# Optimization experiments

Hardware: AMD Instinct MI355X
Metric: run time of the kernel (lower is better)

## Reference

```python
import jax, jax.numpy as jnp
import numpy as np

N = 100_000   # nodes
E = 600_000   # edges
D = 128       # embed_dim
G = 1000      # graphs (batch ids)
L = 3         # num_layers


def setup_inputs() -> dict:
    key = jax.random.key(0)
    ks = jax.random.split(key, 12)
    s = 1.0 / np.sqrt(D)
    return {
        "x": jax.random.normal(ks[0], (N, D), jnp.float32),
        "edge_index": jax.random.randint(ks[1], (2, E), 0, N),
        "batch": jnp.sort(jax.random.randint(ks[2], (N,), 0, G)),
        "mask": jax.random.randint(ks[3], (N,), 0, 2),
        # stacked GCNConv weights/biases (in=hidden=out=D)
        "gcn_w": jax.random.normal(ks[4], (L, D, D), jnp.float32) * s,
        "gcn_b": jnp.zeros((L, D), jnp.float32),
        # MLP head: Linear(D,D) -> ReLU -> Linear(D,1)
        "lin1_w": jax.random.normal(ks[5], (D, D), jnp.float32) * s,
        "lin1_b": jnp.zeros((D,), jnp.float32),
        "lin2_w": jax.random.normal(ks[6], (D,), jnp.float32) * s,
        "lin2_b": jnp.zeros((), jnp.float32),
    }


def gcn_forward(x, src, dst, gcn_w, gcn_b):
    # symmetric gcn_norm with self-loops: deg[i] = 1 + in-degree(i)
    deg = jax.ops.segment_sum(jnp.ones((E,), x.dtype), dst, num_segments=N) + 1.0
    dinv = jax.lax.rsqrt(deg)
    enorm = dinv[src] * dinv[dst]          # [E] edge normalization
    self_norm = (dinv * dinv)[:, None]     # [N,1] self-loop normalization
    h = x
    for l in range(L):
        h = h @ gcn_w[l]                   # [N,D]
        h = (jax.ops.segment_sum(h[src] * enorm[:, None], dst, num_segments=N)
             + h * self_norm)
        h = h + gcn_b[l]
        if l < L - 1:
            h = jax.nn.relu(h)  # (dropout inactive at inference)
    return h


def reference(x, edge_index, batch, mask, gcn_w, gcn_b, lin1_w, lin1_b, lin2_w, lin2_b):
    src, dst = edge_index[0], edge_index[1]
    h = gcn_forward(x, src, dst, gcn_w, gcn_b)
    # MLP head -> per-node score [N]
    s = jax.nn.relu(h @ lin1_w + lin1_b) @ lin2_w + lin2_b
    s = jnp.where(mask == 0, jnp.float32(-1e9), s)
    # per-graph (segment) softmax — fused replacement for the unique/batch loop
    m = jax.ops.segment_max(s, batch, num_segments=G)
    e = jnp.exp(s - m[batch])
    z = jax.ops.segment_sum(e, batch, num_segments=G)
    return e / z[batch]
```

## Files before the change

### kernel.cpp

```cpp
#include <hip/hip_runtime.h>
#include <hip/hip_bf16.h>

typedef unsigned int u32;
typedef unsigned short u16;
typedef __attribute__((ext_vector_type(8))) short bf16x8;
typedef __attribute__((ext_vector_type(4))) float f32x4;

__device__ __forceinline__ float u16tof(u16 u){ return __uint_as_float(((u32)u) << 16); }
__device__ __forceinline__ float lo16(u32 v){ return __uint_as_float(v << 16); }
__device__ __forceinline__ float hi16(u32 v){ return __uint_as_float(v & 0xffff0000u); }
__device__ __forceinline__ u16 ftobf(float f){
  u32 b = __float_as_uint(f);
  return (u16)((b + 0x7FFFu + ((b >> 16) & 1u)) >> 16);
}
__device__ __forceinline__ u32 pack2(float a, float b){
  return (u32)ftobf(a) | ((u32)ftobf(b) << 16);
}
__device__ __forceinline__ float ldf(const void* p, int i, int isbf){
  return isbf ? u16tof(((const u16*)p)[i]) : ((const float*)p)[i];
}

__global__ __launch_bounds__(256) void k_prep(const void* __restrict__ gw, const void* __restrict__ l1w,
                                              const void* __restrict__ x, u16* __restrict__ Wf,
                                              u16* __restrict__ Hb, int L, int n8, int cvtB, int goffB,
                                              const int* __restrict__ batch, int* __restrict__ goff,
                                              int N, int G,
                                              const int* __restrict__ dst, int* __restrict__ bcnt,
                                              int nE, int chunk, int* __restrict__ flag){
  __shared__ int sh[256];
  const int b = blockIdx.x;
  const int t = threadIdx.x;
  const int histStart = L + 1 + cvtB + goffB;

  if (b >= histStart){
    sh[t] = 0; __syncthreads();
    const int blk = b - histStart;
    const int e0 = blk * chunk, e1 = min(e0 + chunk, nE);
    for (int e = e0 + t; e < e1; e += 256) atomicAdd(&sh[dst[e] >> 9], 1);
    __syncthreads();
    if (sh[t] > 0) atomicAdd(&bcnt[t], sh[t]);
    return;
  }
  if (b >= L + 1 + cvtB){
    const int i = (b - (L + 1 + cvtB)) * 256 + t;
    if (i >= N) return;
    const int bt = batch[i];
    const int prev = (i == 0) ? -1 : batch[i - 1];
    for (int g = prev + 1; g <= bt; ++g) goff[g] = i;
    if (i == N - 1){ for (int g = bt + 1; g <= G; ++g) goff[g] = N; }
    return;
  }
  if (t == 0) sh[0] = 0;
  __syncthreads();
  if (b <= L){
    int local = 0;
    for (int i = t; i < 4096; i += 256){
      u32 e = (((const u32*)gw)[i] >> 7) & 0xFFu;
      if (e >= 100u && e < 127u) local++;
    }
    atomicAdd(&sh[0], local);
    __syncthreads();
    const int isbf = (sh[0] > 2048) ? 1 : 0;
    if (b == 0 && t == 0) *flag = isbf;

    const void* src = (b < L) ? gw : l1w;
    const int sbase = (b < L) ? b * 16384 : 0;
    u16* dstp = Wf + (size_t)b * 16384;
    for (int g = t; g < 2048; g += 256){
      const int tt = g >> 8, ks = (g >> 6) & 3, lane = g & 63;
      const int n = tt * 16 + (lane & 15);
      const int k0 = ks * 32 + ((lane >> 4) << 3);
      u16* d = dstp + (size_t)g * 8;
      #pragma unroll
      for (int j = 0; j < 8; ++j){
        d[j] = ftobf(ldf(src, sbase + (k0 + j) * 128 + n, isbf));
      }
    }
  } else {
    u32 e = (((const u32*)gw)[t] >> 7) & 0xFFu;
    atomicAdd(&sh[0], (e >= 100u && e < 127u) ? 1 : 0);
    __syncthreads();
    if (sh[0] > 128) return;
    const int i = (b - (L + 1)) * 256 + t;
    if (i >= n8) return;
    const float4 a = ((const float4*)x)[i * 2];
    const float4 c = ((const float4*)x)[i * 2 + 1];
    u16* o = Hb + (size_t)i * 8;
    o[0] = ftobf(a.x); o[1] = ftobf(a.y); o[2] = ftobf(a.z); o[3] = ftobf(a.w);
    o[4] = ftobf(c.x); o[5] = ftobf(c.y); o[6] = ftobf(c.z); o[7] = ftobf(c.w);
  }
}

__global__ __launch_bounds__(256) void k_bbscan(const int* __restrict__ bcnt, int* __restrict__ bb,
                                                int* __restrict__ bpos, int nE){
  __shared__ int sm[256];
  const int t = threadIdx.x;
  const int v = bcnt[t];
  sm[t] = v; __syncthreads();
  for (int off = 1; off < 256; off <<= 1){
    int a = (t >= off) ? sm[t - off] : 0;
    __syncthreads();
    sm[t] += a;
    __syncthreads();
  }
  const int ex = sm[t] - v;
  bb[t] = ex;
  bpos[t] = ex;
  if (t == 255) bb[256] = nE;
}

__global__ __launch_bounds__(256) void k_scatter(const int* __restrict__ src, const int* __restrict__ dst,
                                                 int* __restrict__ bpos, int2* __restrict__ tmpe,
                                                 int nE, int chunk){
  __shared__ int cnt[256];
  __shared__ int base[256];
  const int blk = blockIdx.x, t = threadIdx.x;
  cnt[t] = 0;
  __syncthreads();
  const int e0 = blk * chunk, e1 = min(e0 + chunk, nE);
  for (int e = e0 + t; e < e1; e += 256) atomicAdd(&cnt[dst[e] >> 9], 1);
  __syncthreads();
  if (cnt[t] > 0) base[t] = atomicAdd(&bpos[t], cnt[t]);
  __syncthreads();
  for (int e = e0 + t; e < e1; e += 256){
    const int d = dst[e];
    const int pos = atomicAdd(&base[d >> 9], 1);
    tmpe[pos] = make_int2(src[e], d);
  }
}

__global__ __launch_bounds__(256) void k_local(const int2* __restrict__ tmpe, const int* __restrict__ bb,
                                               int* __restrict__ boff, int* __restrict__ eid,
                                               float* __restrict__ dinv, int N, int nE, int nbkt){
  __shared__ int hcnt[512];
  __shared__ int hoff[512];
  const int b = blockIdx.x, t = threadIdx.x;
  const int n0 = b << 9;
  const int n1 = min(n0 + 512, N);
  const int nn = n1 - n0;
  const int e0 = bb[b], e1 = bb[b + 1];
  hcnt[t] = 0; hcnt[t + 256] = 0;
  __syncthreads();
  for (int e = e0 + t; e < e1; e += 256) atomicAdd(&hcnt[tmpe[e].y - n0], 1);
  __syncthreads();
  const int v0 = hcnt[t], v1 = hcnt[t + 256];
  hoff[t] = v0; hoff[t + 256] = v1;
  __syncthreads();
  for (int off = 1; off < 512; off <<= 1){
    int a0 = (t >= off) ? hoff[t - off] : 0;
    int a1 = (t + 256 >= off) ? hoff[t + 256 - off] : 0;
    __syncthreads();
    hoff[t] += a0; hoff[t + 256] += a1;
    __syncthreads();
  }
  const int ex0 = hoff[t] - v0 + e0;
  const int ex1 = hoff[t + 256] - v1 + e0;
  if (t < nn){       boff[n0 + t] = ex0;        dinv[n0 + t] = rsqrtf((float)v0 + 1.0f); }
  if (t + 256 < nn){ boff[n0 + t + 256] = ex1;  dinv[n0 + t + 256] = rsqrtf((float)v1 + 1.0f); }
  if (b == nbkt - 1 && t == 0) boff[N] = nE;
  __syncthreads();
  hoff[t] = ex0; hoff[t + 256] = ex1;
  __syncthreads();
  for (int e = e0 + t; e < e1; e += 256){
    const int2 pr = tmpe[e];
    const int pos = atomicAdd(&hoff[pr.y - n0], 1);
    eid[pos] = pr.x;
  }
}

__global__ __launch_bounds__(256) void k_mm(const void* __restrict__ X, const u16* __restrict__ Hb, int use_x,
                                            const u16* __restrict__ Wf, const float* __restrict__ dinv,
                                            u16* __restrict__ T, int n, const int* __restrict__ fl){
  __shared__ u16 smw[16384];
  const int isbf = *fl;
  const u16* A = (use_x && isbf) ? (const u16*)X : Hb;
  {
    const uint4* s = (const uint4*)Wf;
    uint4* d = (uint4*)smw;
    for (int i = threadIdx.x; i < 2048; i += 256) d[i] = s[i];
  }
  __syncthreads();

  const int wave = threadIdx.x >> 6, lane = threadIdx.x & 63;
  const int m0 = blockIdx.x * 64 + wave * 16;
  int arow = m0 + (lane & 15); if (arow > n - 1) arow = n - 1;
  const u16* aptr = A + (size_t)arow * 128 + ((lane >> 4) << 3);

  f32x4 acc[8];
  #pragma unroll
  for (int t = 0; t < 8; ++t) acc[t] = (f32x4){0.f, 0.f, 0.f, 0.f};

  #pragma unroll
  for (int ks = 0; ks < 4; ++ks){
    const bf16x8 a = *(const bf16x8*)(aptr + ks * 32);
    #pragma unroll
    for (int t = 0; t < 8; ++t){
      const bf16x8 b = *(const bf16x8*)(smw + (size_t)(((t * 4 + ks) * 64 + lane) * 8));
      acc[t] = __builtin_amdgcn_mfma_f32_16x16x32_bf16(a, b, acc[t], 0, 0, 0);
    }
  }
  __syncthreads();

  const int quad = lane >> 4, col0 = lane & 15;
  float dv[4];
  #pragma unroll
  for (int r = 0; r < 4; ++r){
    const int row = m0 + quad * 4 + r;
    dv[r] = (row < n) ? dinv[row] : 0.f;
  }
  u16* my = smw + wave * 2112;
  #pragma unroll
  for (int t = 0; t < 8; ++t){
    #pragma unroll
    for (int r = 0; r < 4; ++r){
      my[(quad * 4 + r) * 132 + t * 16 + col0] = ftobf(acc[t][r] * dv[r]);
    }
  }
  #pragma unroll
  for (int i = 0; i < 4; ++i){
    const int row = i * 4 + (lane >> 4);
    const int grow = m0 + row;
    const int c8 = (lane & 15) * 8;
    if (grow < n){
      const u16* s = &my[row * 132 + c8];
      uint2 lo = *(const uint2*)(s);
      uint2 hi = *(const uint2*)(s + 4);
      *(uint4*)&T[(size_t)grow * 128 + c8] = make_uint4(lo.x, lo.y, hi.x, hi.y);
    }
  }
}

__global__ __launch_bounds__(256) void k_mmhead(const u16* __restrict__ Hb, const u16* __restrict__ Wf,
                                                const void* __restrict__ b1, const void* __restrict__ w2,
                                                const void* __restrict__ b2, const int* __restrict__ mask,
                                                float* __restrict__ s, int n, const int* __restrict__ fl){
  __shared__ u16 smw[16384];
  const int isbf = *fl;
  {
    const uint4* sp = (const uint4*)Wf;
    uint4* d = (uint4*)smw;
    for (int i = threadIdx.x; i < 2048; i += 256) d[i] = sp[i];
  }
  __syncthreads();

  const int wave = threadIdx.x >> 6, lane = threadIdx.x & 63;
  const int m0 = blockIdx.x * 64 + wave * 16;
  int arow = m0 + (lane & 15); if (arow > n - 1) arow = n - 1;
  const u16* aptr = Hb + (size_t)arow * 128 + ((lane >> 4) << 3);

  f32x4 acc[8];
  #pragma unroll
  for (int t = 0; t < 8; ++t) acc[t] = (f32x4){0.f, 0.f, 0.f, 0.f};

  #pragma unroll
  for (int ks = 0; ks < 4; ++ks){
    const bf16x8 a = *(const bf16x8*)(aptr + ks * 32);
    #pragma unroll
    for (int t = 0; t < 8; ++t){
      const bf16x8 b = *(const bf16x8*)(smw + (size_t)(((t * 4 + ks) * 64 + lane) * 8));
      acc[t] = __builtin_amdgcn_mfma_f32_16x16x32_bf16(a, b, acc[t], 0, 0, 0);
    }
  }

  const int quad = lane >> 4, col0 = lane & 15;
  float rs0 = 0.f, rs1 = 0.f, rs2 = 0.f, rs3 = 0.f;
  #pragma unroll
  for (int t = 0; t < 8; ++t){
    const int col = t * 16 + col0;
    const float bv = ldf(b1, col, isbf);
    const float wv = ldf(w2, col, isbf);
    rs0 = fmaf(fmaxf(acc[t][0] + bv, 0.f), wv, rs0);
    rs1 = fmaf(fmaxf(acc[t][1] + bv, 0.f), wv, rs1);
    rs2 = fmaf(fmaxf(acc[t][2] + bv, 0.f), wv, rs2);
    rs3 = fmaf(fmaxf(acc[t][3] + bv, 0.f), wv, rs3);
  }
  #pragma unroll
  for (int k = 1; k < 16; k <<= 1){
    rs0 += __shfl_xor(rs0, k);
    rs1 += __shfl_xor(rs1, k);
    rs2 += __shfl_xor(rs2, k);
    rs3 += __shfl_xor(rs3, k);
  }
  if (col0 < 4){
    const int row = m0 + quad * 4 + col0;
    if (row < n){
      float sc = (col0 == 0 ? rs0 : col0 == 1 ? rs1 : col0 == 2 ? rs2 : rs3) + ldf(b2, 0, isbf);
      if (mask[row] == 0) sc = -1e9f;
      s[row] = sc;
    }
  }
}

__global__ __launch_bounds__(256) void k_gather(const u16* __restrict__ T, const int* __restrict__ boff,
                                                const int* __restrict__ eid, const float* __restrict__ dinv,
                                                const void* __restrict__ bias, int layer,
                                                u16* __restrict__ H, int n, int relu,
                                                const int* __restrict__ fl){
  const int wave = threadIdx.x >> 6, lane = threadIdx.x & 63;
  const int sub = lane >> 4, l16 = lane & 15;
  const int node = blockIdx.x * 16 + wave * 4 + sub;
  if (node >= n) return;
  const int isbf = *fl;
  const float di = dinv[node];
  const uint4 sv = ((const uint4*)(T + (size_t)node * 128))[l16];
  float acc0 = lo16(sv.x), acc1 = hi16(sv.x), acc2 = lo16(sv.y), acc3 = hi16(sv.y);
  float acc4 = lo16(sv.z), acc5 = hi16(sv.z), acc6 = lo16(sv.w), acc7 = hi16(sv.w);

  int j = boff[node];
  const int b1 = boff[node + 1];
  for (; j + 4 <= b1; j += 4){
    const int s0 = eid[j], s1 = eid[j + 1], s2 = eid[j + 2], s3 = eid[j + 3];
    const uint4 v0 = ((const uint4*)(T + (size_t)s0 * 128))[l16];
    const uint4 v1 = ((const uint4*)(T + (size_t)s1 * 128))[l16];
    const uint4 v2 = ((const uint4*)(T + (size_t)s2 * 128))[l16];
    const uint4 v3 = ((const uint4*)(T + (size_t)s3 * 128))[l16];
    acc0 += (lo16(v0.x) + lo16(v1.x)) + (lo16(v2.x) + lo16(v3.x));
    acc1 += (hi16(v0.x) + hi16(v1.x)) + (hi16(v2.x) + hi16(v3.x));
    acc2 += (lo16(v0.y) + lo16(v1.y)) + (lo16(v2.y) + lo16(v3.y));
    acc3 += (hi16(v0.y) + hi16(v1.y)) + (hi16(v2.y) + hi16(v3.y));
    acc4 += (lo16(v0.z) + lo16(v1.z)) + (lo16(v2.z) + lo16(v3.z));
    acc5 += (hi16(v0.z) + hi16(v1.z)) + (hi16(v2.z) + hi16(v3.z));
    acc6 += (lo16(v0.w) + lo16(v1.w)) + (lo16(v2.w) + lo16(v3.w));
    acc7 += (hi16(v0.w) + hi16(v1.w)) + (hi16(v2.w) + hi16(v3.w));
  }
  for (; j < b1; ++j){
    const uint4 v = ((const uint4*)(T + (size_t)eid[j] * 128))[l16];
    acc0 += lo16(v.x); acc1 += hi16(v.x);
    acc2 += lo16(v.y); acc3 += hi16(v.y);
    acc4 += lo16(v.z); acc5 += hi16(v.z);
    acc6 += lo16(v.w); acc7 += hi16(v.w);
  }
  const int bb = layer * 128 + l16 * 8;
  float h0 = fmaf(acc0, di, ldf(bias, bb + 0, isbf));
  float h1 = fmaf(acc1, di, ldf(bias, bb + 1, isbf));
  float h2 = fmaf(acc2, di, ldf(bias, bb + 2, isbf));
  float h3 = fmaf(acc3, di, ldf(bias, bb + 3, isbf));
  float h4 = fmaf(acc4, di, ldf(bias, bb + 4, isbf));
  float h5 = fmaf(acc5, di, ldf(bias, bb + 5, isbf));
  float h6 = fmaf(acc6, di, ldf(bias, bb + 6, isbf));
  float h7 = fmaf(acc7, di, ldf(bias, bb + 7, isbf));
  if (relu){
    h0 = fmaxf(h0, 0.f); h1 = fmaxf(h1, 0.f); h2 = fmaxf(h2, 0.f); h3 = fmaxf(h3, 0.f);
    h4 = fmaxf(h4, 0.f); h5 = fmaxf(h5, 0.f); h6 = fmaxf(h6, 0.f); h7 = fmaxf(h7, 0.f);
  }
  uint4 o;
  o.x = pack2(h0, h1); o.y = pack2(h2, h3); o.z = pack2(h4, h5); o.w = pack2(h6, h7);
  ((uint4*)(H + (size_t)node * 128))[l16] = o;
}

__global__ __launch_bounds__(256) void k_gsm(const float* __restrict__ s, const int* __restrict__ goff,
                                             void* __restrict__ out, int G, const int* __restrict__ fl){
  const int g = blockIdx.x * 4 + (threadIdx.x >> 6);
  if (g >= G) return;
  const int lane = threadIdx.x & 63;
  const int i0 = goff[g], i1 = goff[g + 1];
  if (i0 >= i1) return;
  float m = -3.4e38f;
  for (int j = i0 + lane; j < i1; j += 64) m = fmaxf(m, s[j]);
  #pragma unroll
  for (int k = 32; k; k >>= 1) m = fmaxf(m, __shfl_xor(m, k));
  float zz = 0.f;
  for (int j = i0 + lane; j < i1; j += 64) zz += expf(s[j] - m);
  #pragma unroll
  for (int k = 32; k; k >>= 1) zz += __shfl_xor(zz, k);
  const float rz = 1.f / zz;
  const int isbf = *fl;
  for (int j = i0 + lane; j < i1; j += 64){
    const float v = expf(s[j] - m) * rz;
    if (isbf) ((u16*)out)[j] = ftobf(v);
    else      ((float*)out)[j] = v;
  }
}

extern "C" void kernel_launch(void* const* d_in, const int* in_sizes, int n_in,
                              void* d_out, int out_size, void* d_ws, size_t ws_size,
                              hipStream_t stream){
  const void* x    = d_in[0];
  const int* ei    = (const int*)d_in[1];
  const int* batch = (const int*)d_in[2];
  const int* mask  = (const int*)d_in[3];
  const void* gw   = d_in[4];
  const void* gb   = d_in[5];
  const void* l1w  = d_in[6];
  const void* l1b  = d_in[7];
  const void* l2w  = d_in[8];
  const void* l2b  = d_in[9];

  const int N = in_sizes[2];
  const int E = in_sizes[1] / 2;
  const int D = 128;
  const int L = in_sizes[4] / (D * D);
  const int G = 1000;

  char* p = (char*)d_ws;
  u16*  Hb    = (u16*)p;   p += (size_t)N * D * sizeof(u16);
  u16*  Tb    = (u16*)p;   p += (size_t)N * D * sizeof(u16);
  u16*  Wf    = (u16*)p;   p += (size_t)(L + 1) * D * D * sizeof(u16);
  float* dinv = (float*)p; p += (size_t)N * sizeof(float);
  float* sbuf = (float*)p; p += (size_t)N * sizeof(float);
  int*  boff  = (int*)p;   p += (size_t)(N + 1) * sizeof(int);
  int*  eid   = (int*)p;   p += (size_t)E * sizeof(int);
  int*  goff  = (int*)p;   p += (size_t)(G + 1) * sizeof(int);
  int*  bcnt  = (int*)p;   p += 256 * sizeof(int);
  int*  bb    = (int*)p;   p += 260 * sizeof(int);
  int*  bpos  = (int*)p;   p += 256 * sizeof(int);
  int2* tmpe  = (int2*)p;  p += (size_t)E * sizeof(int2);
  int*  flag  = (int*)p;   p += 256;

  const int* srcp = ei;
  const int* dstp = ei + E;

  const int mmg  = (N + 63) / 64;
  const int ndg  = (N + 15) / 16;
  const int n8   = N * D / 8;
  const int cvtB = (n8 + 255) / 256;
  const int goffB = (N + 255) / 256;
  const int chunk = (E + 255) / 256;
  const int nbkt  = (N + 511) / 512;

  hipMemsetAsync(bcnt, 0, 256 * sizeof(int), stream);

  k_prep<<<(L + 1) + cvtB + goffB + 256, 256, 0, stream>>>(gw, l1w, x, Wf, Hb, L, n8, cvtB, goffB,
                                                           batch, goff, N, G, dstp, bcnt, E, chunk, flag);
  k_bbscan<<<1, 256, 0, stream>>>(bcnt, bb, bpos, E);
  k_scatter<<<256, 256, 0, stream>>>(srcp, dstp, bpos, tmpe, E, chunk);
  k_local<<<nbkt, 256, 0, stream>>>(tmpe, bb, boff, eid, dinv, N, E, nbkt);

  for (int l = 0; l < L; ++l){
    k_mm<<<mmg, 256, 0, stream>>>(x, Hb, (l == 0) ? 1 : 0, Wf + (size_t)l * D * D, dinv, Tb, N, flag);
    k_gather<<<ndg, 256, 0, stream>>>(Tb, boff, eid, dinv, gb, l, Hb, N, (l < L - 1) ? 1 : 0, flag);
  }
  k_mmhead<<<mmg, 256, 0, stream>>>(Hb, Wf + (size_t)L * D * D, l1b, l2w, l2b, mask, sbuf, N, flag);
  k_gsm<<<(G + 3) / 4, 256, 0, stream>>>(sbuf, goff, d_out, G, flag);
}
```

Measured before the change: 347.0 us.

## Fuse neighbor gather with next-layer matmul and head; fold bucket scan into scatter

Each GCN aggregation step is fused with the following layer's dense transform (and the last with the MLP head). A 16-node tile is gathered, normalized and ReLU'd into shared memory, then multiplied by the next weight matrix with MFMA, so the intermediate H never round-trips through global memory. The single-block bucket scan kernel is removed by recomputing the 256-entry prefix sum redundantly inside the scatter and local kernels, using a separate zeroed offset counter. The trade-off is that every 16-row block reloads the full 32 KB weight matrix into shared memory, and the small MFMA tiles leave the matmul underused.

```diff
diff --git a/kernel.cpp b/kernel.cpp
--- a/kernel.cpp
+++ b/kernel.cpp
@@ -91,36 +91,28 @@
   }
 }
 
-__global__ __launch_bounds__(256) void k_bbscan(const int* __restrict__ bcnt, int* __restrict__ bb,
-                                                int* __restrict__ bpos, int nE){
+__global__ __launch_bounds__(256) void k_scatter(const int* __restrict__ src, const int* __restrict__ dst,
+                                                 const int* __restrict__ bcnt, int* __restrict__ bpos0,
+                                                 int2* __restrict__ tmpe, int nE, int chunk){
   __shared__ int sm[256];
-  const int t = threadIdx.x;
-  const int v = bcnt[t];
-  sm[t] = v; __syncthreads();
-  for (int off = 1; off < 256; off <<= 1){
-    int a = (t >= off) ? sm[t - off] : 0;
-    __syncthreads();
-    sm[t] += a;
-    __syncthreads();
-  }
-  const int ex = sm[t] - v;
-  bb[t] = ex;
-  bpos[t] = ex;
-  if (t == 255) bb[256] = nE;
-}
-
-__global__ __launch_bounds__(256) void k_scatter(const int* __restrict__ src, const int* __restrict__ dst,
-                                                 int* __restrict__ bpos, int2* __restrict__ tmpe,
-                                                 int nE, int chunk){
   __shared__ int cnt[256];
   __shared__ int base[256];
   const int blk = blockIdx.x, t = threadIdx.x;
+  const int v = bcnt[t];
+  sm[t] = v;
   cnt[t] = 0;
   __syncthreads();
+  for (int off = 1; off < 256; off <<= 1){
+    int a = (t >= off) ? sm[t - off] : 0;
+    __syncthreads();
+    sm[t] += a;
+    __syncthreads();
+  }
+  const int ex = sm[t] - v;
   const int e0 = blk * chunk, e1 = min(e0 + chunk, nE);
   for (int e = e0 + t; e < e1; e += 256) atomicAdd(&cnt[dst[e] >> 9], 1);
   __syncthreads();
-  if (cnt[t] > 0) base[t] = atomicAdd(&bpos[t], cnt[t]);
+  if (cnt[t] > 0) base[t] = ex + atomicAdd(&bpos0[t], cnt[t]);
   __syncthreads();
   for (int e = e0 + t; e < e1; e += 256){
     const int d = dst[e];
@@ -129,16 +121,26 @@
   }
 }
 
-__global__ __launch_bounds__(256) void k_local(const int2* __restrict__ tmpe, const int* __restrict__ bb,
+__global__ __launch_bounds__(256) void k_local(const int2* __restrict__ tmpe, const int* __restrict__ bcnt,
                                                int* __restrict__ boff, int* __restrict__ eid,
                                                float* __restrict__ dinv, int N, int nE, int nbkt){
+  __shared__ int sm[256];
   __shared__ int hcnt[512];
   __shared__ int hoff[512];
   const int b = blockIdx.x, t = threadIdx.x;
+  sm[t] = bcnt[t];
+  __syncthreads();
+  for (int off = 1; off < 256; off <<= 1){
+    int a = (t >= off) ? sm[t - off] : 0;
+    __syncthreads();
+    sm[t] += a;
+    __syncthreads();
+  }
+  const int e0 = (b == 0) ? 0 : sm[b - 1];
+  const int e1 = sm[b];
   const int n0 = b << 9;
   const int n1 = min(n0 + 512, N);
   const int nn = n1 - n0;
-  const int e0 = bb[b], e1 = bb[b + 1];
   hcnt[t] = 0; hcnt[t + 256] = 0;
   __syncthreads();
   for (int e = e0 + t; e < e1; e += 256) atomicAdd(&hcnt[tmpe[e].y - n0], 1);
@@ -168,12 +170,12 @@
   }
 }
 
-__global__ __launch_bounds__(256) void k_mm(const void* __restrict__ X, const u16* __restrict__ Hb, int use_x,
+__global__ __launch_bounds__(256) void k_mm(const void* __restrict__ X, const u16* __restrict__ Hb,
                                             const u16* __restrict__ Wf, const float* __restrict__ dinv,
                                             u16* __restrict__ T, int n, const int* __restrict__ fl){
   __shared__ u16 smw[16384];
   const int isbf = *fl;
-  const u16* A = (use_x && isbf) ? (const u16*)X : Hb;
+  const u16* A = isbf ? (const u16*)X : Hb;
   {
     const uint4* s = (const uint4*)Wf;
     uint4* d = (uint4*)smw;
@@ -230,122 +232,230 @@
   }
 }
 
-__global__ __launch_bounds__(256) void k_mmhead(const u16* __restrict__ Hb, const u16* __restrict__ Wf,
-                                                const void* __restrict__ b1, const void* __restrict__ w2,
-                                                const void* __restrict__ b2, const int* __restrict__ mask,
-                                                float* __restrict__ s, int n, const int* __restrict__ fl){
+__global__ __launch_bounds__(256) void k_gmm(const u16* __restrict__ Tin, const int* __restrict__ boff,
+                                             const int* __restrict__ eid, const float* __restrict__ dinv,
+                                             const void* __restrict__ bias, int layer,
+                                             const u16* __restrict__ Wf, u16* __restrict__ Tout,
+                                             int n, const int* __restrict__ fl){
   __shared__ u16 smw[16384];
+  __shared__ u16 sma[16 * 132];
   const int isbf = *fl;
+  const int wave = threadIdx.x >> 6, lane = threadIdx.x & 63;
+  const int sub = lane >> 4, l16 = lane & 15;
+  const int m0 = blockIdx.x * 16;
+
+  {
+    const uint4* s = (const uint4*)Wf;
+    uint4* d = (uint4*)smw;
+    for (int i = threadIdx.x; i < 2048; i += 256) d[i] = s[i];
+  }
+
+  const int node = m0 + wave * 4 + sub;
+  float h0=0,h1=0,h2=0,h3=0,h4=0,h5=0,h6=0,h7=0;
+  if (node < n){
+    const uint4 sv = ((const uint4*)(Tin + (size_t)node * 128))[l16];
+    float a0 = lo16(sv.x), a1 = hi16(sv.x), a2 = lo16(sv.y), a3 = hi16(sv.y);
+    float a4 = lo16(sv.z), a5 = hi16(sv.z), a6 = lo16(sv.w), a7 = hi16(sv.w);
+    int j = boff[node];
+    const int b1e = boff[node + 1];
+    for (; j + 4 <= b1e; j += 4){
+      const int s0 = eid[j], s1 = eid[j + 1], s2 = eid[j + 2], s3 = eid[j + 3];
+      const uint4 v0 = ((const uint4*)(Tin + (size_t)s0 * 128))[l16];
+      const uint4 v1 = ((const uint4*)(Tin + (size_t)s1 * 128))[l16];
+      const uint4 v2 = ((const uint4*)(Tin + (size_t)s2 * 128))[l16];
+      const uint4 v3 = ((const uint4*)(Tin + (size_t)s3 * 128))[l16];
+      a0 += (lo16(v0.x) + lo16(v1.x)) + (lo16(v2.x) + lo16(v3.x));
+      a1 += (hi16(v0.x) + hi16(v1.x)) + (hi16(v2.x) + hi16(v3.x));
+      a2 += (lo16(v0.y) + lo16(v1.y)) + (lo16(v2.y) + lo16(v3.y));
+      a3 += (hi16(v0.y) + hi16(v1.y)) + (hi16(v2.y) + hi16(v3.y));
+      a4 += (lo16(v0.z) + lo16(v1.z)) + (lo16(v2.z) + lo16(v3.z));
+      a5 += (hi16(v0.z) + hi16(v1.z)) + (hi16(v2.z) + hi16(v3.z));
+      a6 += (lo16(v0.w) + lo16(v1.w)) + (lo16(v2.w) + lo16(v3.w));
+      a7 += (hi16(v0.w) + hi16(v1.w)) + (hi16(v2.w) + hi16(v3.w));
+    }
+    for (; j < b1e; ++j){
+      const uint4 v = ((const uint4*)(Tin + (size_t)eid[j] * 128))[l16];
+      a0 += lo16(v.x); a1 += hi16(v.x);
+      a2 += lo16(v.y); a3 += hi16(v.y);
+      a4 += lo16(v.z); a5 += hi16(v.z);
+      a6 += lo16(v.w); a7 += hi16(v.w);
+    }
+    const float di = dinv[node];
+    const int bb = layer * 128 + l16 * 8;
+    h0 = fmaxf(fmaf(a0, di, ldf(bias, bb + 0, isbf)), 0.f);
+    h1 = fmaxf(fmaf(a1, di, ldf(bias, bb + 1, isbf)), 0.f);
+    h2 = fmaxf(fmaf(a2, di, ldf(bias, bb + 2, isbf)), 0.f);
+    h3 = fmaxf(fmaf(a3, di, ldf(bias, bb + 3, isbf)), 0.f);
+    h4 = fmaxf(fmaf(a4, di, ldf(bias, bb + 4, isbf)), 0.f);
+    h5 = fmaxf(fmaf(a5, di, ldf(bias, bb + 5, isbf)), 0.f);
+    h6 = fmaxf(fmaf(a6, di, ldf(bias, bb + 6, isbf)), 0.f);
+    h7 = fmaxf(fmaf(a7, di, ldf(bias, bb + 7, isbf)), 0.f);
+  }
+  {
+    uint4 o;
+    o.x = pack2(h0, h1); o.y = pack2(h2, h3); o.z = pack2(h4, h5); o.w = pack2(h6, h7);
+    *(uint4*)&sma[(wave * 4 + sub) * 132 + l16 * 8] = o;
+  }
+  __syncthreads();
+
+  f32x4 acc[2];
+  acc[0] = (f32x4){0.f,0.f,0.f,0.f}; acc[1] = (f32x4){0.f,0.f,0.f,0.f};
+  #pragma unroll
+  for (int ks = 0; ks < 4; ++ks){
+    const bf16x8 a = *(const bf16x8*)(sma + l16 * 132 + sub * 8 + ks * 32);
+    #pragma unroll
+    for (int tt = 0; tt < 2; ++tt){
+      const int t = wave * 2 + tt;
+      const bf16x8 b = *(const bf16x8*)(smw + (size_t)(((t * 4 + ks) * 64 + lane) * 8));
+      acc[tt] = __builtin_amdgcn_mfma_f32_16x16x32_bf16(a, b, acc[tt], 0, 0, 0);
+    }
+  }
+  __syncthreads();
+
+  float dv[4];
+  #pragma unroll
+  for (int r = 0; r < 4; ++r){
+    const int row = m0 + sub * 4 + r;
+    dv[r] = (row < n) ? dinv[row] : 0.f;
+  }
+  #pragma unroll
+  for (int tt = 0; tt < 2; ++tt){
+    const int t = wave * 2 + tt;
+    #pragma unroll
+    for (int r = 0; r < 4; ++r){
+      sma[(sub * 4 + r) * 132 + t * 16 + l16] = ftobf(acc[tt][r] * dv[r]);
+    }
+  }
+  __syncthreads();
+
+  {
+    const int row = threadIdx.x >> 4;
+    const int c8 = (threadIdx.x & 15) * 8;
+    if (m0 + row < n){
+      const u16* s = &sma[row * 132 + c8];
+      uint2 lo = *(const uint2*)(s);
+      uint2 hi = *(const uint2*)(s + 4);
+      *(uint4*)&Tout[(size_t)(m0 + row) * 128 + c8] = make_uint4(lo.x, lo.y, hi.x, hi.y);
+    }
+  }
+}
+
+__global__ __launch_bounds__(256) void k_ghead(const u16* __restrict__ Tin, const int* __restrict__ boff,
+                                               const int* __restrict__ eid, const float* __restrict__ dinv,
+                                               const void* __restrict__ bias, int layer,
+                                               const u16* __restrict__ Wf, const void* __restrict__ b1,
+                                               const void* __restrict__ w2, const void* __restrict__ b2,
+                                               const int* __restrict__ mask, float* __restrict__ s,
+                                               int n, const int* __restrict__ fl){
+  __shared__ u16 smw[16384];
+  __shared__ u16 sma[16 * 132];
+  __shared__ float sred[4][16];
+  const int isbf = *fl;
+  const int wave = threadIdx.x >> 6, lane = threadIdx.x & 63;
+  const int sub = lane >> 4, l16 = lane & 15;
+  const int m0 = blockIdx.x * 16;
+
   {
     const uint4* sp = (const uint4*)Wf;
     uint4* d = (uint4*)smw;
     for (int i = threadIdx.x; i < 2048; i += 256) d[i] = sp[i];
   }
-  __syncthreads();
-
-  const int wave = threadIdx.x >> 6, lane = threadIdx.x & 63;
-  const int m0 = blockIdx.x * 64 + wave * 16;
-  int arow = m0 + (lane & 15); if (arow > n - 1) arow = n - 1;
-  const u16* aptr = Hb + (size_t)arow * 128 + ((lane >> 4) << 3);
-
-  f32x4 acc[8];
-  #pragma unroll
-  for (int t = 0; t < 8; ++t) acc[t] = (f32x4){0.f, 0.f, 0.f, 0.f};
-
+
+  const int node = m0 + wave * 4 + sub;
+  float h0=0,h1=0,h2=0,h3=0,h4=0,h5=0,h6=0,h7=0;
+  if (node < n){
+    const uint4 sv = ((const uint4*)(Tin + (size_t)node * 128))[l16];
+    float a0 = lo16(sv.x), a1 = hi16(sv.x), a2 = lo16(sv.y), a3 = hi16(sv.y);
+    float a4 = lo16(sv.z), a5 = hi16(sv.z), a6 = lo16(sv.w), a7 = hi16(sv.w);
+    int j = boff[node];
+    const int b1e = boff[node + 1];
+    for (; j + 4 <= b1e; j += 4){
+      const int s0 = eid[j], s1 = eid[j + 1], s2 = eid[j + 2], s3 = eid[j + 3];
+      const uint4 v0 = ((const uint4*)(Tin + (size_t)s0 * 128))[l16];
+      const uint4 v1 = ((const uint4*)(Tin + (size_t)s1 * 128))[l16];
+      const uint4 v2 = ((const uint4*)(Tin + (size_t)s2 * 128))[l16];
+      const uint4 v3 = ((const uint4*)(Tin + (size_t)s3 * 128))[l16];
+      a0 += (lo16(v0.x) + lo16(v1.x)) + (lo16(v2.x) + lo16(v3.x));
+      a1 += (hi16(v0.x) + hi16(v1.x)) + (hi16(v2.x) + hi16(v3.x));
+      a2 += (lo16(v0.y) + lo16(v1.y)) + (lo16(v2.y) + lo16(v3.y));
+      a3 += (hi16(v0.y) + hi16(v1.y)) + (hi16(v2.y) + hi16(v3.y));
+      a4 += (lo16(v0.z) + lo16(v1.z)) + (lo16(v2.z) + lo16(v3.z));
+      a5 += (hi16(v0.z) + hi16(v1.z)) + (hi16(v2.z) + hi16(v3.z));
+      a6 += (lo16(v0.w) + lo16(v1.w)) + (lo16(v2.w) + lo16(v3.w));
+      a7 += (hi16(v0.w) + hi16(v1.w)) + (hi16(v2.w) + hi16(v3.w));
+    }
+    for (; j < b1e; ++j){
+      const uint4 v = ((const uint4*)(Tin + (size_t)eid[j] * 128))[l16];
+      a0 += lo16(v.x); a1 += hi16(v.x);
+      a2 += lo16(v.y); a3 += hi16(v.y);
+      a4 += lo16(v.z); a5 += hi16(v.z);
+      a6 += lo16(v.w); a7 += hi16(v.w);
+    }
+    const float di = dinv[node];
+    const int bb = layer * 128 + l16 * 8;
+    h0 = fmaf(a0, di, ldf(bias, bb + 0, isbf));
+    h1 = fmaf(a1, di, ldf(bias, bb + 1, isbf));
+    h2 = fmaf(a2, di, ldf(bias, bb + 2, isbf));
+    h3 = fmaf(a3, di, ldf(bias, bb + 3, isbf));
+    h4 = fmaf(a4, di, ldf(bias, bb + 4, isbf));
+    h5 = fmaf(a5, di, ldf(bias, bb + 5, isbf));
+    h6 = fmaf(a6, di, ldf(bias, bb + 6, isbf));
+    h7 = fmaf(a7, di, ldf(bias, bb + 7, isbf));
+  }
+  {
+    uint4 o;
+    o.x = pack2(h0, h1); o.y = pack2(h2, h3); o.z = pack2(h4, h5); o.w = pack2(h6, h7);
+    *(uint4*)&sma[(wave * 4 + sub) * 132 + l16 * 8] = o;
+  }
+  __syncthreads();
+
+  f32x4 acc[2];
+  acc[0] = (f32x4){0.f,0.f,0.f,0.f}; acc[1] = (f32x4){0.f,0.f,0.f,0.f};
   #pragma unroll
   for (int ks = 0; ks < 4; ++ks){
-    const bf16x8 a = *(const bf16x8*)(aptr + ks * 32);
+    const bf16x8 a = *(const bf16x8*)(sma + l16 * 132 + sub * 8 + ks * 32);
     #pragma unroll
-    for (int t = 0; t < 8; ++t){
+    for (int tt = 0; tt < 2; ++tt){
+      const int t = wave * 2 + tt;
       const bf16x8 b = *(const bf16x8*)(smw + (size_t)(((t * 4 + ks) * 64 + lane) * 8));
-      acc[t] = __builtin_amdgcn_mfma_f32_16x16x32_bf16(a, b, acc[t], 0, 0, 0);
-    }
-  }
-
-  const int quad = lane >> 4, col0 = lane & 15;
-  float rs0 = 0.f, rs1 = 0.f, rs2 = 0.f, rs3 = 0.f;
-  #pragma unroll
-  for (int t = 0; t < 8; ++t){
-    const int col = t * 16 + col0;
+      acc[tt] = __builtin_amdgcn_mfma_f32_16x16x32_bf16(a, b, acc[tt], 0, 0, 0);
+    }
+  }
+
+  float p0 = 0.f, p1 = 0.f, p2 = 0.f, p3 = 0.f;
+  #pragma unroll
+  for (int tt = 0; tt < 2; ++tt){
+    const int col = (wave * 2 + tt) * 16 + l16;
     const float bv = ldf(b1, col, isbf);
     const float wv = ldf(w2, col, isbf);
-    rs0 = fmaf(fmaxf(acc[t][0] + bv, 0.f), wv, rs0);
-    rs1 = fmaf(fmaxf(acc[t][1] + bv, 0.f), wv, rs1);
-    rs2 = fmaf(fmaxf(acc[t][2] + bv, 0.f), wv, rs2);
-    rs3 = fmaf(fmaxf(acc[t][3] + bv, 0.f), wv, rs3);
+    p0 = fmaf(fmaxf(acc[tt][0] + bv, 0.f), wv, p0);
+    p1 = fmaf(fmaxf(acc[tt][1] + bv, 0.f), wv, p1);
+    p2 = fmaf(fmaxf(acc[tt][2] + bv, 0.f), wv, p2);
+    p3 = fmaf(fmaxf(acc[tt][3] + bv, 0.f), wv, p3);
   }
   #pragma unroll
   for (int k = 1; k < 16; k <<= 1){
-    rs0 += __shfl_xor(rs0, k);
-    rs1 += __shfl_xor(rs1, k);
-    rs2 += __shfl_xor(rs2, k);
-    rs3 += __shfl_xor(rs3, k);
-  }
-  if (col0 < 4){
-    const int row = m0 + quad * 4 + col0;
+    p0 += __shfl_xor(p0, k);
+    p1 += __shfl_xor(p1, k);
+    p2 += __shfl_xor(p2, k);
+    p3 += __shfl_xor(p3, k);
+  }
+  if (l16 == 0){
+    sred[wave][sub * 4 + 0] = p0;
+    sred[wave][sub * 4 + 1] = p1;
+    sred[wave][sub * 4 + 2] = p2;
+    sred[wave][sub * 4 + 3] = p3;
+  }
+  __syncthreads();
+  if (threadIdx.x < 16){
+    const int row = m0 + threadIdx.x;
     if (row < n){
-      float sc = (col0 == 0 ? rs0 : col0 == 1 ? rs1 : col0 == 2 ? rs2 : rs3) + ldf(b2, 0, isbf);
+      float sc = sred[0][threadIdx.x] + sred[1][threadIdx.x] + sred[2][threadIdx.x] + sred[3][threadIdx.x]
+               + ldf(b2, 0, isbf);
       if (mask[row] == 0) sc = -1e9f;
       s[row] = sc;
     }
   }
-}
-
-__global__ __launch_bounds__(256) void k_gather(const u16* __restrict__ T, const int* __restrict__ boff,
-                                                const int* __restrict__ eid, const float* __restrict__ dinv,
-                                                const void* __restrict__ bias, int layer,
-                                                u16* __restrict__ H, int n, int relu,
-                                                const int* __restrict__ fl){
-  const int wave = threadIdx.x >> 6, lane = threadIdx.x & 63;
-  const int sub = lane >> 4, l16 = lane & 15;
-  const int node = blockIdx.x * 16 + wave * 4 + sub;
-  if (node >= n) return;
-  const int isbf = *fl;
-  const float di = dinv[node];
-  const uint4 sv = ((const uint4*)(T + (size_t)node * 128))[l16];
-  float acc0 = lo16(sv.x), acc1 = hi16(sv.x), acc2 = lo16(sv.y), acc3 = hi16(sv.y);
-  float acc4 = lo16(sv.z), acc5 = hi16(sv.z), acc6 = lo16(sv.w), acc7 = hi16(sv.w);
-
-  int j = boff[node];
-  const int b1 = boff[node + 1];
-  for (; j + 4 <= b1; j += 4){
-    const int s0 = eid[j], s1 = eid[j + 1], s2 = eid[j + 2], s3 = eid[j + 3];
-    const uint4 v0 = ((const uint4*)(T + (size_t)s0 * 128))[l16];
-    const uint4 v1 = ((const uint4*)(T + (size_t)s1 * 128))[l16];
-    const uint4 v2 = ((const uint4*)(T + (size_t)s2 * 128))[l16];
-    const uint4 v3 = ((const uint4*)(T + (size_t)s3 * 128))[l16];
-    acc0 += (lo16(v0.x) + lo16(v1.x)) + (lo16(v2.x) + lo16(v3.x));
-    acc1 += (hi16(v0.x) + hi16(v1.x)) + (hi16(v2.x) + hi16(v3.x));
-    acc2 += (lo16(v0.y) + lo16(v1.y)) + (lo16(v2.y) + lo16(v3.y));
-    acc3 += (hi16(v0.y) + hi16(v1.y)) + (hi16(v2.y) + hi16(v3.y));
-    acc4 += (lo16(v0.z) + lo16(v1.z)) + (lo16(v2.z) + lo16(v3.z));
-    acc5 += (hi16(v0.z) + hi16(v1.z)) + (hi16(v2.z) + hi16(v3.z));
-    acc6 += (lo16(v0.w) + lo16(v1.w)) + (lo16(v2.w) + lo16(v3.w));
-    acc7 += (hi16(v0.w) + hi16(v1.w)) + (hi16(v2.w) + hi16(v3.w));
-  }
-  for (; j < b1; ++j){
-    const uint4 v = ((const uint4*)(T + (size_t)eid[j] * 128))[l16];
-    acc0 += lo16(v.x); acc1 += hi16(v.x);
-    acc2 += lo16(v.y); acc3 += hi16(v.y);
-    acc4 += lo16(v.z); acc5 += hi16(v.z);
-    acc6 += lo16(v.w); acc7 += hi16(v.w);
-  }
-  const int bb = layer * 128 + l16 * 8;
-  float h0 = fmaf(acc0, di, ldf(bias, bb + 0, isbf));
-  float h1 = fmaf(acc1, di, ldf(bias, bb + 1, isbf));
-  float h2 = fmaf(acc2, di, ldf(bias, bb + 2, isbf));
-  float h3 = fmaf(acc3, di, ldf(bias, bb + 3, isbf));
-  float h4 = fmaf(acc4, di, ldf(bias, bb + 4, isbf));
-  float h5 = fmaf(acc5, di, ldf(bias, bb + 5, isbf));
-  float h6 = fmaf(acc6, di, ldf(bias, bb + 6, isbf));
-  float h7 = fmaf(acc7, di, ldf(bias, bb + 7, isbf));
-  if (relu){
-    h0 = fmaxf(h0, 0.f); h1 = fmaxf(h1, 0.f); h2 = fmaxf(h2, 0.f); h3 = fmaxf(h3, 0.f);
-    h4 = fmaxf(h4, 0.f); h5 = fmaxf(h5, 0.f); h6 = fmaxf(h6, 0.f); h7 = fmaxf(h7, 0.f);
-  }
-  uint4 o;
-  o.x = pack2(h0, h1); o.y = pack2(h2, h3); o.z = pack2(h4, h5); o.w = pack2(h6, h7);
-  ((uint4*)(H + (size_t)node * 128))[l16] = o;
 }
 
 __global__ __launch_bounds__(256) void k_gsm(const float* __restrict__ s, const int* __restrict__ goff,
@@ -402,34 +512,32 @@
   int*  eid   = (int*)p;   p += (size_t)E * sizeof(int);
   int*  goff  = (int*)p;   p += (size_t)(G + 1) * sizeof(int);
   int*  bcnt  = (int*)p;   p += 256 * sizeof(int);
-  int*  bb    = (int*)p;   p += 260 * sizeof(int);
-  int*  bpos  = (int*)p;   p += 256 * sizeof(int);
+  int*  bpos0 = (int*)p;   p += 256 * sizeof(int);
   int2* tmpe  = (int2*)p;  p += (size_t)E * sizeof(int2);
   int*  flag  = (int*)p;   p += 256;
 
   const int* srcp = ei;
   const int* dstp = ei + E;
 
-  const int mmg  = (N + 63) / 64;
-  const int ndg  = (N + 15) / 16;
-  const int n8   = N * D / 8;
-  const int cvtB = (n8 + 255) / 256;
+  const int mmg   = (N + 63) / 64;
+  const int fg    = (N + 15) / 16;
+  const int n8    = N * D / 8;
+  const int cvtB  = (n8 + 255) / 256;
   const int goffB = (N + 255) / 256;
   const int chunk = (E + 255) / 256;
   const int nbkt  = (N + 511) / 512;
 
-  hipMemsetAsync(bcnt, 0, 256 * sizeof(int), stream);
+  hipMemsetAsync(bcnt, 0, 512 * sizeof(int), stream);
 
   k_prep<<<(L + 1) + cvtB + goffB + 256, 256, 0, stream>>>(gw, l1w, x, Wf, Hb, L, n8, cvtB, goffB,
                                                            batch, goff, N, G, dstp, bcnt, E, chunk, flag);
-  k_bbscan<<<1, 256, 0, stream>>>(bcnt, bb, bpos, E);
-  k_scatter<<<256, 256, 0, stream>>>(srcp, dstp, bpos, tmpe, E, chunk);
-  k_local<<<nbkt, 256, 0, stream>>>(tmpe, bb, boff, eid, dinv, N, E, nbkt);
-
-  for (int l = 0; l < L; ++l){
-    k_mm<<<mmg, 256, 0, stream>>>(x, Hb, (l == 0) ? 1 : 0, Wf + (size_t)l * D * D, dinv, Tb, N, flag);
-    k_gather<<<ndg, 256, 0, stream>>>(Tb, boff, eid, dinv, gb, l, Hb, N, (l < L - 1) ? 1 : 0, flag);
-  }
-  k_mmhead<<<mmg, 256, 0, stream>>>(Hb, Wf + (size_t)L * D * D, l1b, l2w, l2b, mask, sbuf, N, flag);
+  k_scatter<<<256, 256, 0, stream>>>(srcp, dstp, bcnt, bpos0, tmpe, E, chunk);
+  k_local<<<nbkt, 256, 0, stream>>>(tmpe, bcnt, boff, eid, dinv, N, E, nbkt);
+
+  k_mm<<<mmg, 256, 0, stream>>>(x, Hb, Wf, dinv, Tb, N, flag);
+  k_gmm<<<fg, 256, 0, stream>>>(Tb, boff, eid, dinv, gb, 0, Wf + (size_t)1 * D * D, Hb, N, flag);
+  k_gmm<<<fg, 256, 0, stream>>>(Hb, boff, eid, dinv, gb, 1, Wf + (size_t)2 * D * D, Tb, N, flag);
+  k_ghead<<<fg, 256, 0, stream>>>(Tb, boff, eid, dinv, gb, 2, Wf + (size_t)L * D * D,
+                                  l1b, l2w, l2b, mask, sbuf, N, flag);
   k_gsm<<<(G + 3) / 4, 256, 0, stream>>>(sbuf, goff, d_out, G, flag);
 }
```

New measurement: 357.7 us. 3.1% more time.
